# Kernel optimization log

Hardware: AMD Instinct MI355X
Metric: run time of the kernel (lower is better)

## Reference

```python
import jax, jax.numpy as jnp
import numpy as np

B, LQ, LK, D, H = 2, 1024, 1024, 1024, 16
DH = D // H


def setup_inputs() -> dict:
    key = jax.random.key(0)
    ks = jax.random.split(key, 14)
    s = 1.0 / np.sqrt(D)
    inp = {
        "q": jax.random.normal(ks[0], (B, LQ, D), jnp.float32),
        "k": jax.random.normal(ks[1], (B, LK, D), jnp.float32),
        "v": jax.random.normal(ks[2], (B, LK, D), jnp.float32),
        "Wq": jax.random.normal(ks[3], (D, D), jnp.float32) * s,
        "bq": jnp.zeros((D,), jnp.float32),
        "Wk": jax.random.normal(ks[4], (D, D), jnp.float32) * s,
        "bk": jnp.zeros((D,), jnp.float32),
        "Wv": jax.random.normal(ks[5], (D, D), jnp.float32) * s,
        "bv": jnp.zeros((D,), jnp.float32),
        "Wo": jax.random.normal(ks[6], (D, D), jnp.float32) * s,
        "bo": jnp.zeros((D,), jnp.float32),
        "logits_bias": jax.random.normal(ks[7], (B, LQ, LK), jnp.float32),
        "key_padding_mask": jax.random.randint(ks[8], (B, LK), 0, 2) > 0,
    }
    return inp


def _split_heads(x):
    b, l, _ = x.shape
    return x.reshape(b, l, H, DH).transpose(0, 2, 1, 3)  # [B,H,L,DH]


def reference(q, k, v, Wq, bq, Wk, bk, Wv, bv, Wo, bo, logits_bias, key_padding_mask):
    qh = _split_heads(q @ Wq.T + bq)  # [B,H,Lq,DH]
    kh = _split_heads(k @ Wk.T + bk)  # [B,H,Lk,DH]
    vh = _split_heads(v @ Wv.T + bv)  # [B,H,Lk,DH]

    neg = jnp.finfo(qh.dtype).min
    # attn_mask = logits_bias broadcast over heads, masked_fill at padded keys
    attn_mask = jnp.where(key_padding_mask[:, None, None, :],
                          neg, logits_bias[:, None, :, :])  # [B,1,Lq,Lk]

    scale = 1.0 / np.sqrt(DH)
    scores = jnp.einsum('bhqd,bhkd->bhqk', qh, kh) * scale + attn_mask
    probs = jax.nn.softmax(scores, axis=-1)
    out = jnp.einsum('bhqk,bhkd->bhqd', probs, vh)  # [B,H,Lq,DH]
    out = out.transpose(0, 2, 1, 3).reshape(q.shape[0], q.shape[1], D)
    return out @ Wo.T + bo
```

## Files before the change

kernel.cpp:

```cpp
#include <hip/hip_runtime.h>


typedef _Float16 half8 __attribute__((ext_vector_type(8)));
typedef _Float16 half4_t __attribute__((ext_vector_type(4)));
typedef float f32x4 __attribute__((ext_vector_type(4)));

#define MFMA16(a, b, c) __builtin_amdgcn_mfma_f32_16x16x32_f16((a), (b), (c), 0, 0, 0)

__device__ __forceinline__ void gload16(const void* g, void* l) {
  __builtin_amdgcn_global_load_lds(
      (const __attribute__((address_space(1))) unsigned int*)g,
      (__attribute__((address_space(3))) unsigned int*)l, 16, 0, 0);
}

__device__ __forceinline__ half8 frag_ld(const _Float16* t, int row, int ck) {
  return *(const half8*)(t + row * 64 + (((ck ^ (row & 7)) << 3)));
}

__global__ __launch_bounds__(256) void cvt_f32_f16(
    const float* __restrict__ q, const float* __restrict__ k, const float* __restrict__ v,
    const float* __restrict__ Wq, const float* __restrict__ Wk,
    const float* __restrict__ Wv, const float* __restrict__ Wo,
    _Float16* __restrict__ q16, _Float16* __restrict__ k16, _Float16* __restrict__ v16,
    _Float16* __restrict__ w16) {
  const int y = blockIdx.y;
  if (y >= 3 && blockIdx.x >= 512) return;
  const float* s;
  _Float16* d;
  const size_t M = (size_t)1024 * 1024;
  switch (y) {
    case 0: s = q;  d = q16; break;
    case 1: s = k;  d = k16; break;
    case 2: s = v;  d = v16; break;
    case 3: s = Wq; d = w16; break;
    case 4: s = Wk; d = w16 + M; break;
    case 5: s = Wv; d = w16 + 2 * M; break;
    default: s = Wo; d = w16 + 3 * M; break;
  }
  const size_t i = ((size_t)blockIdx.x * 256 + threadIdx.x) * 8;
  const float4 a = *(const float4*)(s + i);
  const float4 bvv = *(const float4*)(s + i + 4);
  half8 h;
  h[0] = (_Float16)a.x; h[1] = (_Float16)a.y; h[2] = (_Float16)a.z; h[3] = (_Float16)a.w;
  h[4] = (_Float16)bvv.x; h[5] = (_Float16)bvv.y; h[6] = (_Float16)bvv.z; h[7] = (_Float16)bvv.w;
  *(half8*)(d + i) = h;
}

__global__ __launch_bounds__(256) void mm_bt(
    const _Float16* __restrict__ Aq, const _Float16* __restrict__ Ak,
    const _Float16* __restrict__ Av, const _Float16* __restrict__ W16,
    const float* __restrict__ c0, const float* __restrict__ c1,
    const float* __restrict__ c2, _Float16* __restrict__ Dq,
    _Float16* __restrict__ Dk, _Float16* __restrict__ Dvt,
    float* __restrict__ Df, int is_final) {
  __shared__ __align__(16) _Float16 lds[17408];
  _Float16* As = lds;
  _Float16* Bs = lds + 8192;

  const int tid = threadIdx.x;
  const int wv = tid >> 6, ln = tid & 63;
  const int quad = ln >> 4, col = ln & 15;
  const int wm = wv >> 1, wn = wv & 1;
  const int n0 = blockIdx.x * 128;
  const int m0 = blockIdx.y * 128;
  const int z = blockIdx.z;

  const _Float16* A = (z == 0) ? Aq : (z == 1) ? Ak : Av;
  const _Float16* Bw = W16 + (size_t)z * 1024 * 1024;
  const float* bias = (z == 0) ? c0 : (z == 1) ? c1 : c2;

  const f32x4 zero4 = {0.f, 0.f, 0.f, 0.f};
  f32x4 acc[4][4];
#pragma unroll
  for (int i = 0; i < 4; ++i)
#pragma unroll
    for (int j = 0; j < 4; ++j) acc[i][j] = zero4;

  for (int k0 = 0; k0 < 1024; k0 += 64) {
    __syncthreads();
#pragma unroll
    for (int j = 0; j < 4; ++j) {
      const int ci = j * 256 + wv * 64 + ln;
      const int row = ci >> 3;
      const int lc = (ci & 7) ^ (row & 7);
      gload16(A + (size_t)(m0 + row) * 1024 + k0 + lc * 8,
              As + (size_t)(j * 256 + wv * 64) * 8);
      gload16(Bw + (size_t)(n0 + row) * 1024 + k0 + lc * 8,
              Bs + (size_t)(j * 256 + wv * 64) * 8);
    }
    __syncthreads();
#pragma unroll
    for (int kk = 0; kk < 2; ++kk) {
      half8 af[4], bf[4];
#pragma unroll
      for (int mi = 0; mi < 4; ++mi)
        af[mi] = frag_ld(As, wm * 64 + mi * 16 + col, kk * 4 + quad);
#pragma unroll
      for (int ni = 0; ni < 4; ++ni)
        bf[ni] = frag_ld(Bs, wn * 64 + ni * 16 + col, kk * 4 + quad);
#pragma unroll
      for (int mi = 0; mi < 4; ++mi)
#pragma unroll
        for (int ni = 0; ni < 4; ++ni)
          acc[mi][ni] = MFMA16(af[mi], bf[ni], acc[mi][ni]);
    }
  }

  float bv[4];
#pragma unroll
  for (int ni = 0; ni < 4; ++ni) bv[ni] = bias[n0 + wn * 64 + ni * 16 + col];

  if (is_final) {
#pragma unroll
    for (int mi = 0; mi < 4; ++mi) {
      const int m_g = m0 + wm * 64 + mi * 16 + quad * 4;
#pragma unroll
      for (int ni = 0; ni < 4; ++ni) {
        const int n_g = n0 + wn * 64 + ni * 16 + col;
#pragma unroll
        for (int r = 0; r < 4; ++r)
          Df[(size_t)(m_g + r) * 1024 + n_g] = acc[mi][ni][r] + bv[ni];
      }
    }
  } else if (z < 2) {
    _Float16* D = z ? Dk : Dq;
#pragma unroll
    for (int mi = 0; mi < 4; ++mi) {
      const int m_g = m0 + wm * 64 + mi * 16 + quad * 4;
#pragma unroll
      for (int ni = 0; ni < 4; ++ni) {
        const int n_g = n0 + wn * 64 + ni * 16 + col;
        const int h = n_g >> 6, dh = n_g & 63;
#pragma unroll
        for (int r = 0; r < 4; ++r) {
          const int b = (m_g + r) >> 10, l = (m_g + r) & 1023;
          D[((size_t)((b * 16 + h) * 1024) + l) * 64 + dh] =
              (_Float16)(acc[mi][ni][r] + bv[ni]);
        }
      }
    }
  } else {
    __syncthreads();
    _Float16* Ct = lds;
#pragma unroll
    for (int mi = 0; mi < 4; ++mi) {
      const int ml = wm * 64 + mi * 16 + quad * 4;
#pragma unroll
      for (int ni = 0; ni < 4; ++ni) {
        const int nl = wn * 64 + ni * 16 + col;
#pragma unroll
        for (int r = 0; r < 4; ++r)
          Ct[(size_t)nl * 136 + ml + r] = (_Float16)(acc[mi][ni][r] + bv[ni]);
      }
    }
    __syncthreads();
#pragma unroll
    for (int it = 0; it < 8; ++it) {
      const int ci = it * 256 + tid;
      const int n = ci >> 4;
      const int mc = (ci & 15) * 8;
      const half8 hv = *(const half8*)(Ct + (size_t)n * 136 + mc);
      const int n_g = n0 + n;
      const int h = n_g >> 6, dh = n_g & 63;
      const int m_g = m0 + mc;
      const int b = m_g >> 10, l = m_g & 1023;
      *(half8*)(Dvt + ((size_t)((b * 16 + h) * 64 + dh)) * 1024 + l) = hv;
    }
  }
}

__global__ __launch_bounds__(256) void attn(
    const _Float16* __restrict__ Qh, const _Float16* __restrict__ Kh,
    const _Float16* __restrict__ Vt, const float* __restrict__ biasL,
    const int* __restrict__ kpm, _Float16* __restrict__ AO) {
  __shared__ __align__(16) _Float16 Qs[4096];
  __shared__ __align__(16) _Float16 Ks[4096];
  __shared__ __align__(16) _Float16 Vs[4096];
  __shared__ __align__(16) _Float16 Pt[4096];

  const int tid = threadIdx.x;
  const int wv = tid >> 6, ln = tid & 63;
  const int quad = ln >> 4, col = ln & 15;
  const int q0 = blockIdx.x * 64;
  const int bh = blockIdx.y;
  const int b = bh >> 4, hh = bh & 15;
  const int qg = q0 + wv * 16 + col;

#pragma unroll
  for (int j = 0; j < 2; ++j) {
    const int ci = j * 256 + wv * 64 + ln;
    const int row = ci >> 3;
    const int lc = (ci & 7) ^ (row & 7);
    gload16(Qh + ((size_t)bh * 1024 + q0 + row) * 64 + lc * 8,
            Qs + (size_t)(j * 256 + wv * 64) * 8);
  }
  __syncthreads();
  const half8 bq0 = frag_ld(Qs, wv * 16 + col, quad);
  const half8 bq1 = frag_ld(Qs, wv * 16 + col, 4 + quad);

  const f32x4 zero4 = {0.f, 0.f, 0.f, 0.f};
  f32x4 o[4];
#pragma unroll
  for (int ni = 0; ni < 4; ++ni) o[ni] = zero4;
  float m_i = -1e30f, l_i = 0.f;

  _Float16* Pw = Pt + wv * 1024;

  for (int k0 = 0; k0 < 1024; k0 += 64) {
    __syncthreads();
#pragma unroll
    for (int j = 0; j < 2; ++j) {
      const int ci = j * 256 + wv * 64 + ln;
      const int row = ci >> 3;
      const int lc = (ci & 7) ^ (row & 7);
      gload16(Kh + ((size_t)bh * 1024 + k0 + row) * 64 + lc * 8,
              Ks + (size_t)(j * 256 + wv * 64) * 8);
      gload16(Vt + ((size_t)(bh * 64 + row)) * 1024 + k0 + lc * 8,
              Vs + (size_t)(j * 256 + wv * 64) * 8);
    }
    f32x4 bb[4];
    int4 mk4[4];
#pragma unroll
    for (int mi = 0; mi < 4; ++mi) {
      const int kg = k0 + mi * 16 + quad * 4;
      mk4[mi] = *(const int4*)&kpm[b * 1024 + kg];
      bb[mi] = *(const f32x4*)&biasL[((size_t)(b * 1024 + qg)) * 1024 + kg];
    }
    __syncthreads();

    f32x4 s[4];
#pragma unroll
    for (int mi = 0; mi < 4; ++mi) {
      f32x4 a4 = zero4;
      a4 = MFMA16(frag_ld(Ks, mi * 16 + col, quad), bq0, a4);
      a4 = MFMA16(frag_ld(Ks, mi * 16 + col, 4 + quad), bq1, a4);
      s[mi] = a4;
    }
#pragma unroll
    for (int mi = 0; mi < 4; ++mi) {
      const int* mp = (const int*)&mk4[mi];
#pragma unroll
      for (int r = 0; r < 4; ++r)
        s[mi][r] = mp[r] ? -1e9f : s[mi][r] * 0.125f + bb[mi][r];
    }

    float rm = -1e30f;
#pragma unroll
    for (int mi = 0; mi < 4; ++mi)
#pragma unroll
      for (int r = 0; r < 4; ++r) rm = fmaxf(rm, s[mi][r]);
    rm = fmaxf(rm, __shfl_xor(rm, 16));
    rm = fmaxf(rm, __shfl_xor(rm, 32));
    const float mn = fmaxf(m_i, rm);
    const float alpha = __expf(m_i - mn);
    m_i = mn;
    float ps = 0.f;
#pragma unroll
    for (int mi = 0; mi < 4; ++mi)
#pragma unroll
      for (int r = 0; r < 4; ++r) {
        const float p = __expf(s[mi][r] - mn);
        s[mi][r] = p;
        ps += p;
      }
    ps += __shfl_xor(ps, 16);
    ps += __shfl_xor(ps, 32);
    l_i = l_i * alpha + ps;
#pragma unroll
    for (int ni = 0; ni < 4; ++ni)
#pragma unroll
      for (int r = 0; r < 4; ++r) o[ni][r] *= alpha;

#pragma unroll
    for (int mi = 0; mi < 4; ++mi) {
      half4_t h;
      h[0] = (_Float16)s[mi][0]; h[1] = (_Float16)s[mi][1];
      h[2] = (_Float16)s[mi][2]; h[3] = (_Float16)s[mi][3];
      const int kloc = mi * 16 + quad * 4;
      const int chunk = kloc >> 3;
      *(half4_t*)(Pw + col * 64 + (((chunk ^ (col & 7)) << 3) | (kloc & 7))) = h;
    }
    const half8 p0 = frag_ld(Pw, col, quad);
    const half8 p1 = frag_ld(Pw, col, 4 + quad);

#pragma unroll
    for (int ni = 0; ni < 4; ++ni) {
      o[ni] = MFMA16(frag_ld(Vs, ni * 16 + col, quad), p0, o[ni]);
      o[ni] = MFMA16(frag_ld(Vs, ni * 16 + col, 4 + quad), p1, o[ni]);
    }
  }

  const float inv = 1.0f / l_i;
#pragma unroll
  for (int ni = 0; ni < 4; ++ni) {
    half4_t h;
#pragma unroll
    for (int r = 0; r < 4; ++r) h[r] = (_Float16)(o[ni][r] * inv);
    *(half4_t*)&AO[((size_t)(b * 1024 + qg)) * 1024 + hh * 64 + ni * 16 + quad * 4] = h;
  }
}

extern "C" void kernel_launch(void* const* d_in, const int* in_sizes, int n_in,
                              void* d_out, int out_size, void* d_ws, size_t ws_size,
                              hipStream_t stream) {
  (void)in_sizes; (void)n_in; (void)out_size; (void)ws_size;
  const float* q = (const float*)d_in[0];
  const float* k = (const float*)d_in[1];
  const float* v = (const float*)d_in[2];
  const float* Wq = (const float*)d_in[3];
  const float* bq = (const float*)d_in[4];
  const float* Wk = (const float*)d_in[5];
  const float* bk = (const float*)d_in[6];
  const float* Wv = (const float*)d_in[7];
  const float* bv = (const float*)d_in[8];
  const float* Wo = (const float*)d_in[9];
  const float* bo = (const float*)d_in[10];
  const float* lb = (const float*)d_in[11];
  const int* kpm = (const int*)d_in[12];
  float* out = (float*)d_out;

  const size_t NT = (size_t)2 * 1024 * 1024;
  _Float16* q16 = (_Float16*)d_ws;
  _Float16* k16 = q16 + NT;
  _Float16* v16 = k16 + NT;
  _Float16* Qh = v16 + NT;
  _Float16* Kh = Qh + NT;
  _Float16* Vt = Kh + NT;
  _Float16* w16 = Vt + NT;
  _Float16* AO = q16;

  cvt_f32_f16<<<dim3(1024, 7), 256, 0, stream>>>(q, k, v, Wq, Wk, Wv, Wo,
                                                 q16, k16, v16, w16);
  mm_bt<<<dim3(8, 16, 3), 256, 0, stream>>>(q16, k16, v16, w16, bq, bk, bv,
                                            Qh, Kh, Vt, nullptr, 0);
  attn<<<dim3(16, 32), 256, 0, stream>>>(Qh, Kh, Vt, lb, kpm, AO);
  mm_bt<<<dim3(8, 16, 1), 256, 0, stream>>>(AO, nullptr, nullptr, w16 + 3 * NT / 2,
                                            bo, nullptr, nullptr, nullptr, nullptr,
                                            nullptr, out, 1);
}
```

Baseline: 185.6 us.

## Split attention KV range across waves and read K/V directly from global

```diff
diff --git a/kernel.cpp b/kernel.cpp
--- a/kernel.cpp
+++ b/kernel.cpp
@@ -169,34 +169,26 @@
   }
 }
 
-__global__ __launch_bounds__(256) void attn(
+__global__ __launch_bounds__(256, 3) void attn(
     const _Float16* __restrict__ Qh, const _Float16* __restrict__ Kh,
     const _Float16* __restrict__ Vt, const float* __restrict__ biasL,
     const int* __restrict__ kpm, _Float16* __restrict__ AO) {
-  __shared__ __align__(16) _Float16 Qs[4096];
-  __shared__ __align__(16) _Float16 Ks[4096];
-  __shared__ __align__(16) _Float16 Vs[4096];
-  __shared__ __align__(16) _Float16 Pt[4096];
+  __shared__ __align__(16) _Float16 Pt[4 * 1024];
+  __shared__ __align__(16) float OxS[2 * 4 * 64 * 4];
+  __shared__ float MlS[2 * 2 * 64];
 
   const int tid = threadIdx.x;
   const int wv = tid >> 6, ln = tid & 63;
   const int quad = ln >> 4, col = ln & 15;
-  const int q0 = blockIdx.x * 64;
+  const int qsub = wv & 1, khalf = wv >> 1;
+  const int q0 = blockIdx.x * 32;
   const int bh = blockIdx.y;
   const int b = bh >> 4, hh = bh & 15;
-  const int qg = q0 + wv * 16 + col;
-
-#pragma unroll
-  for (int j = 0; j < 2; ++j) {
-    const int ci = j * 256 + wv * 64 + ln;
-    const int row = ci >> 3;
-    const int lc = (ci & 7) ^ (row & 7);
-    gload16(Qh + ((size_t)bh * 1024 + q0 + row) * 64 + lc * 8,
-            Qs + (size_t)(j * 256 + wv * 64) * 8);
-  }
-  __syncthreads();
-  const half8 bq0 = frag_ld(Qs, wv * 16 + col, quad);
-  const half8 bq1 = frag_ld(Qs, wv * 16 + col, 4 + quad);
+  const int qg = q0 + qsub * 16 + col;
+
+  const _Float16* Qp = Qh + ((size_t)bh * 1024 + qg) * 64;
+  const half8 bq0 = *(const half8*)(Qp + quad * 8);
+  const half8 bq1 = *(const half8*)(Qp + 32 + quad * 8);
 
   const f32x4 zero4 = {0.f, 0.f, 0.f, 0.f};
   f32x4 o[4];
@@ -205,43 +197,33 @@
   float m_i = -1e30f, l_i = 0.f;
 
   _Float16* Pw = Pt + wv * 1024;
-
-  for (int k0 = 0; k0 < 1024; k0 += 64) {
-    __syncthreads();
-#pragma unroll
-    for (int j = 0; j < 2; ++j) {
-      const int ci = j * 256 + wv * 64 + ln;
-      const int row = ci >> 3;
-      const int lc = (ci & 7) ^ (row & 7);
-      gload16(Kh + ((size_t)bh * 1024 + k0 + row) * 64 + lc * 8,
-              Ks + (size_t)(j * 256 + wv * 64) * 8);
-      gload16(Vt + ((size_t)(bh * 64 + row)) * 1024 + k0 + lc * 8,
-              Vs + (size_t)(j * 256 + wv * 64) * 8);
-    }
-    f32x4 bb[4];
-    int4 mk4[4];
-#pragma unroll
-    for (int mi = 0; mi < 4; ++mi) {
-      const int kg = k0 + mi * 16 + quad * 4;
-      mk4[mi] = *(const int4*)&kpm[b * 1024 + kg];
-      bb[mi] = *(const f32x4*)&biasL[((size_t)(b * 1024 + qg)) * 1024 + kg];
-    }
-    __syncthreads();
+  const _Float16* Kb = Kh + (size_t)bh * 1024 * 64;
+  const _Float16* Vb = Vt + (size_t)bh * 64 * 1024;
+  const float* biasRow = biasL + ((size_t)(b * 1024 + qg)) * 1024;
+  const int* kpmRow = kpm + b * 1024;
+
+  for (int it = 0; it < 8; ++it) {
+    const int koff = khalf * 512 + it * 64;
 
     f32x4 s[4];
 #pragma unroll
     for (int mi = 0; mi < 4; ++mi) {
+      const _Float16* Kp = Kb + (size_t)(koff + mi * 16 + col) * 64;
       f32x4 a4 = zero4;
-      a4 = MFMA16(frag_ld(Ks, mi * 16 + col, quad), bq0, a4);
-      a4 = MFMA16(frag_ld(Ks, mi * 16 + col, 4 + quad), bq1, a4);
+      a4 = MFMA16(*(const half8*)(Kp + quad * 8), bq0, a4);
+      a4 = MFMA16(*(const half8*)(Kp + 32 + quad * 8), bq1, a4);
       s[mi] = a4;
     }
-#pragma unroll
-    for (int mi = 0; mi < 4; ++mi) {
-      const int* mp = (const int*)&mk4[mi];
+
+#pragma unroll
+    for (int mi = 0; mi < 4; ++mi) {
+      const int kg = koff + mi * 16 + quad * 4;
+      const int4 mk4 = *(const int4*)&kpmRow[kg];
+      const f32x4 bb = *(const f32x4*)&biasRow[kg];
+      const int* mp = (const int*)&mk4;
 #pragma unroll
       for (int r = 0; r < 4; ++r)
-        s[mi][r] = mp[r] ? -1e9f : s[mi][r] * 0.125f + bb[mi][r];
+        s[mi][r] = mp[r] ? -1e9f : s[mi][r] * 0.125f + bb[r];
     }
 
     float rm = -1e30f;
@@ -285,18 +267,36 @@
 
 #pragma unroll
     for (int ni = 0; ni < 4; ++ni) {
-      o[ni] = MFMA16(frag_ld(Vs, ni * 16 + col, quad), p0, o[ni]);
-      o[ni] = MFMA16(frag_ld(Vs, ni * 16 + col, 4 + quad), p1, o[ni]);
-    }
-  }
-
-  const float inv = 1.0f / l_i;
-#pragma unroll
-  for (int ni = 0; ni < 4; ++ni) {
-    half4_t h;
-#pragma unroll
-    for (int r = 0; r < 4; ++r) h[r] = (_Float16)(o[ni][r] * inv);
-    *(half4_t*)&AO[((size_t)(b * 1024 + qg)) * 1024 + hh * 64 + ni * 16 + quad * 4] = h;
+      const _Float16* Vp = Vb + (size_t)(ni * 16 + col) * 1024 + koff;
+      o[ni] = MFMA16(*(const half8*)(Vp + quad * 8), p0, o[ni]);
+      o[ni] = MFMA16(*(const half8*)(Vp + 32 + quad * 8), p1, o[ni]);
+    }
+  }
+
+  if (khalf == 1) {
+#pragma unroll
+    for (int ni = 0; ni < 4; ++ni)
+      *(f32x4*)&OxS[((qsub * 4 + ni) * 64 + ln) * 4] = o[ni];
+    MlS[qsub * 128 + ln] = m_i;
+    MlS[qsub * 128 + 64 + ln] = l_i;
+  }
+  __syncthreads();
+  if (khalf == 0) {
+    const float m2 = MlS[qsub * 128 + ln];
+    const float l2 = MlS[qsub * 128 + 64 + ln];
+    const float ms = fmaxf(m_i, m2);
+    const float w1 = __expf(m_i - ms);
+    const float w2 = __expf(m2 - ms);
+    const float inv = 1.0f / (l_i * w1 + l2 * w2);
+#pragma unroll
+    for (int ni = 0; ni < 4; ++ni) {
+      const f32x4 o2 = *(const f32x4*)&OxS[((qsub * 4 + ni) * 64 + ln) * 4];
+      half4_t h;
+#pragma unroll
+      for (int r = 0; r < 4; ++r)
+        h[r] = (_Float16)((o[ni][r] * w1 + o2[r] * w2) * inv);
+      *(half4_t*)&AO[((size_t)(b * 1024 + qg)) * 1024 + hh * 64 + ni * 16 + quad * 4] = h;
+    }
   }
 }
 
@@ -333,7 +333,7 @@
                                                  q16, k16, v16, w16);
   mm_bt<<<dim3(8, 16, 3), 256, 0, stream>>>(q16, k16, v16, w16, bq, bk, bv,
                                             Qh, Kh, Vt, nullptr, 0);
-  attn<<<dim3(16, 32), 256, 0, stream>>>(Qh, Kh, Vt, lb, kpm, AO);
+  attn<<<dim3(32, 32), 256, 0, stream>>>(Qh, Kh, Vt, lb, kpm, AO);
   mm_bt<<<dim3(8, 16, 1), 256, 0, stream>>>(AO, nullptr, nullptr, w16 + 3 * NT / 2,
                                             bo, nullptr, nullptr, nullptr, nullptr,
                                             nullptr, out, 1);
```

Result: slower. 230.1 us (+24.0%).
